# Optimization experiments

Hardware: AMD Instinct MI355X
Metric: run time of the kernel (lower is better)

The kernel has to match this reference:

```python
import jax, jax.numpy as jnp
import numpy as np

B, N, E = 4096, 64, 256      # graph pairs, nodes per drug, directed edges per drug
F, H, FP = 128, 64, 2048     # node feat dim, hidden dim, fingerprint dim


def setup_inputs() -> dict:
    key = jax.random.key(0)
    ks = jax.random.split(key, 14)
    return {
        "x1": jax.random.normal(ks[0], (B, N, F), jnp.float32),
        "x2": jax.random.normal(ks[1], (B, N, F), jnp.float32),
        "edge1": jax.random.randint(ks[2], (B, 2, E), 0, N, jnp.int32),
        "edge2": jax.random.randint(ks[3], (B, 2, E), 0, N, jnp.int32),
        "fp1": jax.random.uniform(ks[4], (B, FP), jnp.float32),
        "fp2": jax.random.uniform(ks[5], (B, FP), jnp.float32),
        "W1": jax.random.normal(ks[6], (F, H), jnp.float32) * 0.05,
        "b1": jnp.zeros((H,), jnp.float32),
        "W2": jax.random.normal(ks[7], (H, H), jnp.float32) * 0.05,
        "b2": jnp.zeros((H,), jnp.float32),
        "Wm1": jax.random.normal(ks[8], (2 * H + 2 * FP, 256), jnp.float32) * 0.02,
        "bm1": jnp.zeros((256,), jnp.float32),
        "Wm2": jax.random.normal(ks[9], (256, 1), jnp.float32) * 0.05,
        "bm2": jnp.zeros((1,), jnp.float32),
    }


def gcn_conv(x, src, dst, W, b):
    """PyG GCNConv: self-loops + symmetric normalization, aggregated at dst."""
    n = x.shape[0]
    loops = jnp.arange(n, dtype=src.dtype)
    s = jnp.concatenate([src, loops])
    d = jnp.concatenate([dst, loops])
    deg = jax.ops.segment_sum(jnp.ones_like(d, jnp.float32), d, num_segments=n)
    norm = jax.lax.rsqrt(deg)                      # deg >= 1 due to self-loops
    xw = x @ W                                     # [n, H]
    msg = xw[s] * (norm[s] * norm[d])[:, None]     # [n+E, H]
    return jax.ops.segment_sum(msg, d, num_segments=n) + b


def encode(x, edges, W1, b1, W2, b2):
    src, dst = edges[0], edges[1]
    h = jax.nn.relu(gcn_conv(x, src, dst, W1, b1))
    h = jax.nn.relu(gcn_conv(h, src, dst, W2, b2))
    return h.mean(axis=0)                          # global_mean_pool (1 graph)


_encode_b = jax.vmap(encode, in_axes=(0, 0, None, None, None, None))


def reference(x1, x2, edge1, edge2, fp1, fp2, W1, b1, W2, b2, Wm1, bm1, Wm2, bm2):
    h1 = _encode_b(x1, edge1, W1, b1, W2, b2)      # [B, H]
    h2 = _encode_b(x2, edge2, W1, b1, W2, b2)      # [B, H]
    fused = jnp.concatenate([h1, h2, fp1, fp2], axis=1)  # [B, 2H+2FP]
    hidden = jax.nn.relu(fused @ Wm1 + bm1)
    return jax.nn.sigmoid(hidden @ Wm2 + bm2).reshape(-1)
```

## Files before the change

kernel.cpp:

```cpp
#include <hip/hip_runtime.h>
#include <math.h>

#define B_PAIRS 4096
#define NNODES  64
#define NEDGES  256
#define FDIM    128
#define HDIM    64
#define FPDIM   2048
#define MDIM    256
#define KTOT    4224

typedef __attribute__((ext_vector_type(4))) float f32x4;
typedef __bf16 bf16x8 __attribute__((ext_vector_type(8)));

__device__ __forceinline__ unsigned short f2bf(float f) {
    return __builtin_bit_cast(unsigned short, (__bf16)f);
}
__device__ __forceinline__ unsigned pack2(float a, float b) {
    return (unsigned)f2bf(a) | ((unsigned)f2bf(b) << 16);
}
__device__ __forceinline__ unsigned long long pack4(float a, float b, float c, float d) {
    return (unsigned long long)pack2(a, b) | ((unsigned long long)pack2(c, d) << 32);
}

__global__ void prep_weights(const float* __restrict__ W1, const float* __restrict__ W2,
                             unsigned short* __restrict__ W1t, unsigned short* __restrict__ W2t) {
    const int t0 = blockIdx.x * 256 + threadIdx.x;
    const int stride = gridDim.x * 256;
    for (int i = t0; i < HDIM * FDIM; i += stride) {
        const int n = i >> 7, k = i & 127;
        W1t[i] = f2bf(W1[k * HDIM + n]);
    }
    for (int i = t0; i < HDIM * HDIM; i += stride) {
        const int n = i >> 6, k = i & 63;
        W2t[i] = f2bf(W2[k * HDIM + n]);
    }
}

__global__ __launch_bounds__(256)
void prep_wm1(const float* __restrict__ Wm1, unsigned short* __restrict__ Wm1t) {
    __shared__ float tile[32][33];
    const int k0 = blockIdx.x * 32, n0 = blockIdx.y * 32;
    const int t = threadIdx.x;
    const int c = t & 31, r8 = t >> 5;
    #pragma unroll
    for (int rr = r8; rr < 32; rr += 8)
        tile[rr][c] = Wm1[(size_t)(k0 + rr) * MDIM + n0 + c];
    __syncthreads();
    #pragma unroll
    for (int j = 0; j < 4; ++j) {
        const int n = n0 + r8 + 8 * j;
        Wm1t[(size_t)n * KTOT + k0 + c] = f2bf(tile[c][r8 + 8 * j]);
    }
}

#define WAITLDS() do { __asm__ volatile("s_waitcnt lgkmcnt(0)" ::: "memory"); \
                       __builtin_amdgcn_sched_barrier(0); } while (0)

__global__ __launch_bounds__(64, 2)
void encode_kernel(const float* __restrict__ x1, const float* __restrict__ x2,
                   const int* __restrict__ e1, const int* __restrict__ e2,
                   const unsigned short* __restrict__ W1t, const float* __restrict__ b1,
                   const unsigned short* __restrict__ W2t, const float* __restrict__ b2,
                   float* __restrict__ hbuf) {
    __shared__ __align__(16) unsigned char lds[17152];
    const int gid  = blockIdx.x;
    const int drug = gid >> 12;
    const int b    = gid & (B_PAIRS - 1);
    const float* x  = (drug ? x2 : x1) + (size_t)b * NNODES * FDIM;
    const int*   eg = (drug ? e2 : e1) + (size_t)b * 2 * NEDGES;

    const int t  = threadIdx.x;
    const int lr = t & 15, lg = t >> 4;
    const unsigned swl = (unsigned)(lr & 7) << 4;

    unsigned* cnt = (unsigned*)(lds + 8192);
    float*    nrm = (float*)(lds + 16640);
    int*      deg = (int*)(lds + 16896);

    float4 xalo[16];
    #pragma unroll
    for (int mt = 0; mt < 2; ++mt) {
        const float* xr = x + (size_t)(16 * mt + lr) * FDIM + 8 * lg;
        #pragma unroll
        for (int ks = 0; ks < 4; ++ks) {
            xalo[mt * 8 + 2 * ks]     = ((const float4*)(xr + 32 * ks))[0];
            xalo[mt * 8 + 2 * ks + 1] = ((const float4*)(xr + 32 * ks))[1];
        }
    }
    const int4 s4 = ((const int4*)eg)[t];
    const int4 d4 = ((const int4*)eg)[t + 64];

    #pragma unroll
    for (int i = 0; i < 8; ++i) ((uint4*)cnt)[t + 64 * i] = make_uint4(0, 0, 0, 0);
    if (t < 16) ((uint4*)cnt)[512 + t] = make_uint4(0, 0, 0, 0);
    deg[t] = 0;
    WAITLDS();

    {
        const int ss[4] = {s4.x, s4.y, s4.z, s4.w};
        const int dd[4] = {d4.x, d4.y, d4.z, d4.w};
        #pragma unroll
        for (int i = 0; i < 4; ++i) {
            atomicAdd(&deg[dd[i]], 1);
            atomicAdd(&cnt[dd[i] * 33 + (ss[i] >> 1)], 1u << ((ss[i] & 1) * 16));
        }
    }
    WAITLDS();

    float4 xahi[16];
    #pragma unroll
    for (int mt = 0; mt < 2; ++mt) {
        const float* xr = x + (size_t)(16 * (mt + 2) + lr) * FDIM + 8 * lg;
        #pragma unroll
        for (int ks = 0; ks < 4; ++ks) {
            xahi[mt * 8 + 2 * ks]     = ((const float4*)(xr + 32 * ks))[0];
            xahi[mt * 8 + 2 * ks + 1] = ((const float4*)(xr + 32 * ks))[1];
        }
    }

    nrm[t] = rsqrtf((float)deg[t] + 1.0f);
    WAITLDS();

    bf16x8 bw1[16];
    #pragma unroll
    for (int nt = 0; nt < 4; ++nt)
        #pragma unroll
        for (int ks = 0; ks < 4; ++ks)
            bw1[nt * 4 + ks] = *(const bf16x8*)(W1t + (16 * nt + lr) * FDIM + 32 * ks + 8 * lg);

    {
        const int r = t;
        const float nr = nrm[r];
        unsigned char* arow = lds + r * 128;
        const unsigned sw = (unsigned)(r & 7) << 4;
        #pragma unroll
        for (int cw = 0; cw < 16; ++cw) {
            const unsigned w0 = cnt[r * 33 + 2 * cw];
            const unsigned w1 = cnt[r * 33 + 2 * cw + 1];
            const float4 nv = ((const float4*)nrm)[cw];
            const int c = 4 * cw;
            const float u0 = (float)((w0 & 0xffffu) + (r == c     ? 1u : 0u)) * nr * nv.x;
            const float u1 = (float)((w0 >> 16)     + (r == c + 1 ? 1u : 0u)) * nr * nv.y;
            const float u2 = (float)((w1 & 0xffffu) + (r == c + 2 ? 1u : 0u)) * nr * nv.z;
            const float u3 = (float)((w1 >> 16)     + (r == c + 3 ? 1u : 0u)) * nr * nv.w;
            *(unsigned long long*)(arow + (((unsigned)(8 * cw)) ^ sw)) = pack4(u0, u1, u2, u3);
        }
    }
    WAITLDS();

    #pragma unroll
    for (int half = 0; half < 2; ++half) {
        const float4* xs = half ? xahi : xalo;
        #pragma unroll
        for (int m2i = 0; m2i < 2; ++m2i) {
            const int mt = half * 2 + m2i;
            f32x4 acc[4];
            #pragma unroll
            for (int nt = 0; nt < 4; ++nt) acc[nt] = (f32x4){0.f, 0.f, 0.f, 0.f};
            #pragma unroll
            for (int ks = 0; ks < 4; ++ks) {
                bf16x8 a;
                const float4 u = xs[m2i * 8 + 2 * ks], v = xs[m2i * 8 + 2 * ks + 1];
                a[0] = (__bf16)u.x; a[1] = (__bf16)u.y; a[2] = (__bf16)u.z; a[3] = (__bf16)u.w;
                a[4] = (__bf16)v.x; a[5] = (__bf16)v.y; a[6] = (__bf16)v.z; a[7] = (__bf16)v.w;
                #pragma unroll
                for (int nt = 0; nt < 4; ++nt)
                    acc[nt] = __builtin_amdgcn_mfma_f32_16x16x32_bf16(a, bw1[nt * 4 + ks], acc[nt], 0, 0, 0);
            }
            const unsigned m2 = (unsigned)(2 * (16 * mt + 4 * lg));
            #pragma unroll
            for (int nt = 0; nt < 4; ++nt) {
                const int f = 16 * nt + lr;
                *(unsigned long long*)(lds + 8192u + (unsigned)f * 128 + (m2 ^ swl)) =
                    pack4(acc[nt][0], acc[nt][1], acc[nt][2], acc[nt][3]);
            }
        }
    }
    WAITLDS();

    {
        bf16x8 ta[8], ba[8];
        #pragma unroll
        for (int mt = 0; mt < 4; ++mt)
            #pragma unroll
            for (int ks = 0; ks < 2; ++ks)
                ta[mt * 2 + ks] = *(const bf16x8*)(lds + 8192u + (unsigned)(16 * mt + lr) * 128 +
                                                   (((unsigned)(64 * ks + 16 * lg)) ^ swl));
        #pragma unroll
        for (int nt = 0; nt < 4; ++nt)
            #pragma unroll
            for (int ks = 0; ks < 2; ++ks)
                ba[nt * 2 + ks] = *(const bf16x8*)(lds + (unsigned)(16 * nt + lr) * 128 +
                                                   (((unsigned)(64 * ks + 16 * lg)) ^ swl));
        WAITLDS();
        #pragma unroll
        for (int mt = 0; mt < 4; ++mt) {
            f32x4 acc[4];
            #pragma unroll
            for (int nt = 0; nt < 4; ++nt) acc[nt] = (f32x4){0.f, 0.f, 0.f, 0.f};
            #pragma unroll
            for (int ks = 0; ks < 2; ++ks) {
                #pragma unroll
                for (int nt = 0; nt < 4; ++nt)
                    acc[nt] = __builtin_amdgcn_mfma_f32_16x16x32_bf16(ta[mt * 2 + ks], ba[nt * 2 + ks], acc[nt], 0, 0, 0);
            }
            const int m0 = 16 * mt + 4 * lg;
            const float4 b1v = *(const float4*)(b1 + m0);
            const unsigned m2 = (unsigned)(2 * m0);
            #pragma unroll
            for (int nt = 0; nt < 4; ++nt) {
                const int d = 16 * nt + lr;
                const float v0 = fmaxf(acc[nt][0] + b1v.x, 0.f);
                const float v1 = fmaxf(acc[nt][1] + b1v.y, 0.f);
                const float v2 = fmaxf(acc[nt][2] + b1v.z, 0.f);
                const float v3 = fmaxf(acc[nt][3] + b1v.w, 0.f);
                *(unsigned long long*)(lds + 8192u + (unsigned)d * 128 + (m2 ^ swl)) =
                    pack4(v0, v1, v2, v3);
            }
        }
    }
    WAITLDS();

    {
        bf16x8 ta[8], bw2[8];
        #pragma unroll
        for (int mt = 0; mt < 4; ++mt)
            #pragma unroll
            for (int ks = 0; ks < 2; ++ks)
                ta[mt * 2 + ks] = *(const bf16x8*)(lds + 8192u + (unsigned)(16 * mt + lr) * 128 +
                                                   (((unsigned)(64 * ks + 16 * lg)) ^ swl));
        #pragma unroll
        for (int nt = 0; nt < 4; ++nt)
            #pragma unroll
            for (int ks = 0; ks < 2; ++ks)
                bw2[nt * 2 + ks] = *(const bf16x8*)(W2t + (16 * nt + lr) * HDIM + 32 * ks + 8 * lg);
        WAITLDS();
        #pragma unroll
        for (int mt = 0; mt < 4; ++mt) {
            f32x4 acc[4];
            #pragma unroll
            for (int nt = 0; nt < 4; ++nt) acc[nt] = (f32x4){0.f, 0.f, 0.f, 0.f};
            #pragma unroll
            for (int ks = 0; ks < 2; ++ks) {
                #pragma unroll
                for (int nt = 0; nt < 4; ++nt)
                    acc[nt] = __builtin_amdgcn_mfma_f32_16x16x32_bf16(ta[mt * 2 + ks], bw2[nt * 2 + ks], acc[nt], 0, 0, 0);
            }
            const unsigned m2 = (unsigned)(2 * (16 * mt + 4 * lg));
            #pragma unroll
            for (int nt = 0; nt < 4; ++nt) {
                const int n = 16 * nt + lr;
                *(unsigned long long*)(lds + 8192u + (unsigned)n * 128 + (m2 ^ swl)) =
                    pack4(acc[nt][0], acc[nt][1], acc[nt][2], acc[nt][3]);
            }
        }
    }
    WAITLDS();

    {
        bf16x8 bt3[8];
        #pragma unroll
        for (int nt = 0; nt < 4; ++nt)
            #pragma unroll
            for (int ks = 0; ks < 2; ++ks)
                bt3[nt * 2 + ks] = *(const bf16x8*)(lds + 8192u + (unsigned)(16 * nt + lr) * 128 +
                                                    (((unsigned)(64 * ks + 16 * lg)) ^ swl));
        float b2v[4], p[4];
        #pragma unroll
        for (int nt = 0; nt < 4; ++nt) { b2v[nt] = b2[16 * nt + lr]; p[nt] = 0.f; }
        #pragma unroll
        for (int mt = 0; mt < 4; ++mt) {
            f32x4 acc[4];
            #pragma unroll
            for (int nt = 0; nt < 4; ++nt) acc[nt] = (f32x4){0.f, 0.f, 0.f, 0.f};
            #pragma unroll
            for (int ks = 0; ks < 2; ++ks) {
                const bf16x8 a = *(const bf16x8*)(lds + (unsigned)(16 * mt + lr) * 128 +
                                                  (((unsigned)(64 * ks + 16 * lg)) ^ swl));
                #pragma unroll
                for (int nt = 0; nt < 4; ++nt)
                    acc[nt] = __builtin_amdgcn_mfma_f32_16x16x32_bf16(a, bt3[nt * 2 + ks], acc[nt], 0, 0, 0);
            }
            #pragma unroll
            for (int nt = 0; nt < 4; ++nt) {
                #pragma unroll
                for (int j = 0; j < 4; ++j) p[nt] += fmaxf(acc[nt][j] + b2v[nt], 0.f);
            }
        }
        #pragma unroll
        for (int nt = 0; nt < 4; ++nt) {
            p[nt] += __shfl_xor(p[nt], 16, 64);
            p[nt] += __shfl_xor(p[nt], 32, 64);
        }
        if (lg == 0) {
            float* hout = hbuf + ((size_t)drug * B_PAIRS + b) * HDIM;
            #pragma unroll
            for (int nt = 0; nt < 4; ++nt) hout[16 * nt + lr] = p[nt] * (1.0f / 64.0f);
        }
    }
}

__global__ __launch_bounds__(256)
void fused_mlp_kernel(const float* __restrict__ fp1, const float* __restrict__ fp2,
                      const float* __restrict__ hbuf,
                      const unsigned short* __restrict__ Wm1t,
                      const float* __restrict__ bm1, const float* __restrict__ Wm2,
                      const float* __restrict__ bm2, float* __restrict__ out) {
    __shared__ __align__(16) unsigned char lds[8448];
    float* pool = (float*)(lds + 8192);
    const int t = threadIdx.x;
    const int lane = t & 63, wid = t >> 6;
    const int lr = lane & 15, lg = lane >> 4;
    const int pair0 = blockIdx.x * 16;

    const int r  = t >> 4;
    const int kc = (t & 15) << 3;
    const int pr = pair0 + r;
    const unsigned wOff = (unsigned)r * 256 + (((unsigned)(2 * kc)) ^ ((unsigned)(r & 7) << 4));

    f32x4 acc[4];
    #pragma unroll
    for (int nf = 0; nf < 4; ++nf) acc[nf] = (f32x4){0.f, 0.f, 0.f, 0.f};

    const unsigned short* brow[4];
    #pragma unroll
    for (int nf = 0; nf < 4; ++nf)
        brow[nf] = Wm1t + (size_t)(64 * wid + 16 * nf + lr) * KTOT + 8 * lg;

    float4 va, vb;
    #define LOAD_A(s)                                                                  \
        {                                                                              \
            const float* src;                                                          \
            if ((s) == 0)                                                              \
                src = (kc < 64) ? hbuf + (size_t)pr * HDIM + kc                        \
                                : hbuf + (size_t)(B_PAIRS + pr) * HDIM + (kc - 64);    \
            else if ((s) <= 16)                                                        \
                src = fp1 + (size_t)pr * FPDIM + ((s) - 1) * 128 + kc;                 \
            else                                                                       \
                src = fp2 + (size_t)pr * FPDIM + ((s) - 17) * 128 + kc;                \
            va = ((const float4*)src)[0];                                              \
            vb = ((const float4*)src)[1];                                              \
        }
    #define STORE_A(base)                                                              \
        *(uint4*)((base) + wOff) = make_uint4(pack2(va.x, va.y), pack2(va.z, va.w),    \
                                              pack2(vb.x, vb.y), pack2(vb.z, vb.w));

    LOAD_A(0);
    STORE_A(lds);
    for (int s = 0; s < 33; ++s) {
        const bool more = (s + 1 < 33);
        if (more) LOAD_A(s + 1);
        __syncthreads();
        const unsigned char* buf = lds + (unsigned)((s & 1) << 12);
        const unsigned asw = (unsigned)(lr & 7) << 4;
        const int kglob = s << 7;
        #pragma unroll
        for (int ks = 0; ks < 4; ++ks) {
            const unsigned kb = (unsigned)(64 * ks + 16 * lg);
            const bf16x8 a = *(const bf16x8*)(buf + (unsigned)lr * 256 + (kb ^ asw));
            #pragma unroll
            for (int nf = 0; nf < 4; ++nf) {
                const bf16x8 bw = *(const bf16x8*)(brow[nf] + kglob + 32 * ks);
                acc[nf] = __builtin_amdgcn_mfma_f32_16x16x32_bf16(a, bw, acc[nf], 0, 0, 0);
            }
        }
        if (more) STORE_A(lds + (unsigned)(((s + 1) & 1) << 12));
    }

    float bm1v[4], wm2v[4];
    #pragma unroll
    for (int nf = 0; nf < 4; ++nf) {
        const int n = 64 * wid + 16 * nf + lr;
        bm1v[nf] = bm1[n];
        wm2v[nf] = Wm2[n];
    }
    #pragma unroll
    for (int reg = 0; reg < 4; ++reg) {
        float p = 0.f;
        #pragma unroll
        for (int nf = 0; nf < 4; ++nf)
            p += fmaxf(acc[nf][reg] + bm1v[nf], 0.f) * wm2v[nf];
        p += __shfl_xor(p, 1, 64);
        p += __shfl_xor(p, 2, 64);
        p += __shfl_xor(p, 4, 64);
        p += __shfl_xor(p, 8, 64);
        if (lr == 0) pool[wid * 16 + 4 * lg + reg] = p;
    }
    __syncthreads();
    if (t < 16) {
        const float y = pool[t] + pool[16 + t] + pool[32 + t] + pool[48 + t] + bm2[0];
        out[pair0 + t] = 1.0f / (1.0f + expf(-y));
    }
    #undef LOAD_A
    #undef STORE_A
}

extern "C" void kernel_launch(void* const* d_in, const int* in_sizes, int n_in,
                              void* d_out, int out_size, void* d_ws, size_t ws_size,
                              hipStream_t stream) {
    const float* x1  = (const float*)d_in[0];
    const float* x2  = (const float*)d_in[1];
    const int*   e1  = (const int*)d_in[2];
    const int*   e2  = (const int*)d_in[3];
    const float* fp1 = (const float*)d_in[4];
    const float* fp2 = (const float*)d_in[5];
    const float* W1  = (const float*)d_in[6];
    const float* b1  = (const float*)d_in[7];
    const float* W2  = (const float*)d_in[8];
    const float* b2  = (const float*)d_in[9];
    const float* Wm1 = (const float*)d_in[10];
    const float* bm1 = (const float*)d_in[11];
    const float* Wm2 = (const float*)d_in[12];
    const float* bm2 = (const float*)d_in[13];
    float* out  = (float*)d_out;

    float* hbuf = (float*)d_ws;
    unsigned short* W1t  = (unsigned short*)((char*)d_ws + (2 << 20));
    unsigned short* W2t  = W1t + HDIM * FDIM;
    unsigned short* Wm1t = (unsigned short*)((char*)d_ws + (3 << 20));

    hipLaunchKernelGGL(prep_weights, dim3(16), dim3(256), 0, stream, W1, W2, W1t, W2t);
    hipLaunchKernelGGL(prep_wm1, dim3(132, 8), dim3(256), 0, stream, Wm1, Wm1t);
    hipLaunchKernelGGL(encode_kernel, dim3(2 * B_PAIRS), dim3(64), 0, stream,
                       x1, x2, e1, e2, W1t, b1, W2t, b2, hbuf);
    hipLaunchKernelGGL(fused_mlp_kernel, dim3(B_PAIRS / 16), dim3(256), 0, stream,
                       fp1, fp2, hbuf, Wm1t, bm1, Wm2, bm2, out);
}
```

Baseline: 162.3 us.

## Process four graphs per encode block with software-prefetched node features

The encode kernel becomes persistent-ish: each 64-thread block loops over four graphs instead of one, hoisting W2/b2 loads out of the loop. While the current graph is computed, the next graph's node features and edge lists are prefetched into registers, so global load latency overlaps with MFMA and LDS work. The cost is fewer blocks (2048 instead of 8192), which lowers parallelism and latency hiding across waves, plus higher register pressure from the double-buffered feature registers under launch_bounds(64,2).

```diff
diff --git a/kernel.cpp b/kernel.cpp
--- a/kernel.cpp
+++ b/kernel.cpp
@@ -9,6 +9,7 @@
 #define FPDIM   2048
 #define MDIM    256
 #define KTOT    4224
+#define GPW     4
 
 typedef __attribute__((ext_vector_type(4))) float f32x4;
 typedef __bf16 bf16x8 __attribute__((ext_vector_type(8)));
@@ -21,6 +22,12 @@
 }
 __device__ __forceinline__ unsigned long long pack4(float a, float b, float c, float d) {
     return (unsigned long long)pack2(a, b) | ((unsigned long long)pack2(c, d) << 32);
+}
+__device__ __forceinline__ bf16x8 cvt8(float4 u, float4 v) {
+    bf16x8 a;
+    a[0] = (__bf16)u.x; a[1] = (__bf16)u.y; a[2] = (__bf16)u.z; a[3] = (__bf16)u.w;
+    a[4] = (__bf16)v.x; a[5] = (__bf16)v.y; a[6] = (__bf16)v.z; a[7] = (__bf16)v.w;
+    return a;
 }
 
 __global__ void prep_weights(const float* __restrict__ W1, const float* __restrict__ W2,
@@ -64,12 +71,6 @@
                    const unsigned short* __restrict__ W2t, const float* __restrict__ b2,
                    float* __restrict__ hbuf) {
     __shared__ __align__(16) unsigned char lds[17152];
-    const int gid  = blockIdx.x;
-    const int drug = gid >> 12;
-    const int b    = gid & (B_PAIRS - 1);
-    const float* x  = (drug ? x2 : x1) + (size_t)b * NNODES * FDIM;
-    const int*   eg = (drug ? e2 : e1) + (size_t)b * 2 * NEDGES;
-
     const int t  = threadIdx.x;
     const int lr = t & 15, lg = t >> 4;
     const unsigned swl = (unsigned)(lr & 7) << 4;
@@ -78,96 +79,137 @@
     float*    nrm = (float*)(lds + 16640);
     int*      deg = (int*)(lds + 16896);
 
-    float4 xalo[16];
-    #pragma unroll
-    for (int mt = 0; mt < 2; ++mt) {
-        const float* xr = x + (size_t)(16 * mt + lr) * FDIM + 8 * lg;
-        #pragma unroll
-        for (int ks = 0; ks < 4; ++ks) {
-            xalo[mt * 8 + 2 * ks]     = ((const float4*)(xr + 32 * ks))[0];
-            xalo[mt * 8 + 2 * ks + 1] = ((const float4*)(xr + 32 * ks))[1];
-        }
-    }
-    const int4 s4 = ((const int4*)eg)[t];
-    const int4 d4 = ((const int4*)eg)[t + 64];
-
-    #pragma unroll
-    for (int i = 0; i < 8; ++i) ((uint4*)cnt)[t + 64 * i] = make_uint4(0, 0, 0, 0);
-    if (t < 16) ((uint4*)cnt)[512 + t] = make_uint4(0, 0, 0, 0);
-    deg[t] = 0;
-    WAITLDS();
-
+    const int g0 = blockIdx.x * GPW;
+
+    bf16x8 bw2[8];
+    #pragma unroll
+    for (int nt = 0; nt < 4; ++nt)
+        #pragma unroll
+        for (int ks = 0; ks < 2; ++ks)
+            bw2[nt * 2 + ks] = *(const bf16x8*)(W2t + (16 * nt + lr) * HDIM + 32 * ks + 8 * lg);
+    float b2v[4];
+    #pragma unroll
+    for (int nt = 0; nt < 4; ++nt) b2v[nt] = b2[16 * nt + lr];
+
+    float4 xaA[16], xaB[16];
+    int4 s4, d4;
     {
-        const int ss[4] = {s4.x, s4.y, s4.z, s4.w};
-        const int dd[4] = {d4.x, d4.y, d4.z, d4.w};
-        #pragma unroll
-        for (int i = 0; i < 4; ++i) {
-            atomicAdd(&deg[dd[i]], 1);
-            atomicAdd(&cnt[dd[i] * 33 + (ss[i] >> 1)], 1u << ((ss[i] & 1) * 16));
-        }
-    }
-    WAITLDS();
-
-    float4 xahi[16];
-    #pragma unroll
-    for (int mt = 0; mt < 2; ++mt) {
-        const float* xr = x + (size_t)(16 * (mt + 2) + lr) * FDIM + 8 * lg;
-        #pragma unroll
-        for (int ks = 0; ks < 4; ++ks) {
-            xahi[mt * 8 + 2 * ks]     = ((const float4*)(xr + 32 * ks))[0];
-            xahi[mt * 8 + 2 * ks + 1] = ((const float4*)(xr + 32 * ks))[1];
-        }
-    }
-
-    nrm[t] = rsqrtf((float)deg[t] + 1.0f);
-    WAITLDS();
-
-    bf16x8 bw1[16];
-    #pragma unroll
-    for (int nt = 0; nt < 4; ++nt)
-        #pragma unroll
-        for (int ks = 0; ks < 4; ++ks)
-            bw1[nt * 4 + ks] = *(const bf16x8*)(W1t + (16 * nt + lr) * FDIM + 32 * ks + 8 * lg);
-
-    {
-        const int r = t;
-        const float nr = nrm[r];
-        unsigned char* arow = lds + r * 128;
-        const unsigned sw = (unsigned)(r & 7) << 4;
-        #pragma unroll
-        for (int cw = 0; cw < 16; ++cw) {
-            const unsigned w0 = cnt[r * 33 + 2 * cw];
-            const unsigned w1 = cnt[r * 33 + 2 * cw + 1];
-            const float4 nv = ((const float4*)nrm)[cw];
-            const int c = 4 * cw;
-            const float u0 = (float)((w0 & 0xffffu) + (r == c     ? 1u : 0u)) * nr * nv.x;
-            const float u1 = (float)((w0 >> 16)     + (r == c + 1 ? 1u : 0u)) * nr * nv.y;
-            const float u2 = (float)((w1 & 0xffffu) + (r == c + 2 ? 1u : 0u)) * nr * nv.z;
-            const float u3 = (float)((w1 >> 16)     + (r == c + 3 ? 1u : 0u)) * nr * nv.w;
-            *(unsigned long long*)(arow + (((unsigned)(8 * cw)) ^ sw)) = pack4(u0, u1, u2, u3);
-        }
-    }
-    WAITLDS();
-
-    #pragma unroll
-    for (int half = 0; half < 2; ++half) {
-        const float4* xs = half ? xahi : xalo;
-        #pragma unroll
-        for (int m2i = 0; m2i < 2; ++m2i) {
-            const int mt = half * 2 + m2i;
+        const int gid = g0;
+        const float* x = ((gid >> 12) ? x2 : x1) + (size_t)(gid & (B_PAIRS - 1)) * NNODES * FDIM;
+        #pragma unroll
+        for (int mt = 0; mt < 2; ++mt) {
+            const float* xr = x + (size_t)(16 * mt + lr) * FDIM + 8 * lg;
+            #pragma unroll
+            for (int ks = 0; ks < 4; ++ks) {
+                xaA[mt * 8 + 2 * ks]     = ((const float4*)(xr + 32 * ks))[0];
+                xaA[mt * 8 + 2 * ks + 1] = ((const float4*)(xr + 32 * ks))[1];
+            }
+            const float* xr2 = x + (size_t)(16 * (mt + 2) + lr) * FDIM + 8 * lg;
+            #pragma unroll
+            for (int ks = 0; ks < 4; ++ks) {
+                xaB[mt * 8 + 2 * ks]     = ((const float4*)(xr2 + 32 * ks))[0];
+                xaB[mt * 8 + 2 * ks + 1] = ((const float4*)(xr2 + 32 * ks))[1];
+            }
+        }
+        const int* eg = ((gid >> 12) ? e2 : e1) + (size_t)(gid & (B_PAIRS - 1)) * 2 * NEDGES;
+        s4 = ((const int4*)eg)[t];
+        d4 = ((const int4*)eg)[t + 64];
+    }
+
+    #pragma unroll 1
+    for (int it = 0; it < GPW; ++it) {
+        const int gid  = g0 + it;
+        const int drug = gid >> 12;
+        const int b    = gid & (B_PAIRS - 1);
+        const bool more = (it + 1 < GPW);
+        const int gn   = gid + 1;
+        const float* xn = ((gn >> 12) ? x2 : x1) + (size_t)(gn & (B_PAIRS - 1)) * NNODES * FDIM;
+        const int*  egn = ((gn >> 12) ? e2 : e1) + (size_t)(gn & (B_PAIRS - 1)) * 2 * NEDGES;
+
+        #pragma unroll
+        for (int i = 0; i < 8; ++i) ((uint4*)cnt)[t + 64 * i] = make_uint4(0, 0, 0, 0);
+        if (t < 16) ((uint4*)cnt)[512 + t] = make_uint4(0, 0, 0, 0);
+        deg[t] = 0;
+        WAITLDS();
+
+        {
+            const int ss[4] = {s4.x, s4.y, s4.z, s4.w};
+            const int dd[4] = {d4.x, d4.y, d4.z, d4.w};
+            #pragma unroll
+            for (int i = 0; i < 4; ++i) {
+                atomicAdd(&deg[dd[i]], 1);
+                atomicAdd(&cnt[dd[i] * 33 + (ss[i] >> 1)], 1u << ((ss[i] & 1) * 16));
+            }
+        }
+        WAITLDS();
+        nrm[t] = rsqrtf((float)deg[t] + 1.0f);
+        WAITLDS();
+
+        bf16x8 bw1[16];
+        #pragma unroll
+        for (int nt = 0; nt < 4; ++nt)
+            #pragma unroll
+            for (int ks = 0; ks < 4; ++ks)
+                bw1[nt * 4 + ks] = *(const bf16x8*)(W1t + (16 * nt + lr) * FDIM + 32 * ks + 8 * lg);
+
+        {
+            const int r = t;
+            const float nr = nrm[r];
+            unsigned char* arow = lds + r * 128;
+            const unsigned sw = (unsigned)(r & 7) << 4;
+            #pragma unroll
+            for (int cw = 0; cw < 16; ++cw) {
+                const unsigned w0 = cnt[r * 33 + 2 * cw];
+                const unsigned w1 = cnt[r * 33 + 2 * cw + 1];
+                const float4 nv = ((const float4*)nrm)[cw];
+                const int c = 4 * cw;
+                const float u0 = (float)((w0 & 0xffffu) + (r == c     ? 1u : 0u)) * nr * nv.x;
+                const float u1 = (float)((w0 >> 16)     + (r == c + 1 ? 1u : 0u)) * nr * nv.y;
+                const float u2 = (float)((w1 & 0xffffu) + (r == c + 2 ? 1u : 0u)) * nr * nv.z;
+                const float u3 = (float)((w1 >> 16)     + (r == c + 3 ? 1u : 0u)) * nr * nv.w;
+                *(unsigned long long*)(arow + (((unsigned)(8 * cw)) ^ sw)) = pack4(u0, u1, u2, u3);
+            }
+        }
+        WAITLDS();
+
+        bf16x8 xb[16];
+        #pragma unroll
+        for (int mt = 0; mt < 2; ++mt)
+            #pragma unroll
+            for (int ks = 0; ks < 4; ++ks)
+                xb[mt * 4 + ks] = cvt8(xaA[mt * 8 + 2 * ks], xaA[mt * 8 + 2 * ks + 1]);
+        if (more) {
+            #pragma unroll
+            for (int mt = 0; mt < 2; ++mt) {
+                const float* xr = xn + (size_t)(16 * mt + lr) * FDIM + 8 * lg;
+                #pragma unroll
+                for (int ks = 0; ks < 4; ++ks) {
+                    xaA[mt * 8 + 2 * ks]     = ((const float4*)(xr + 32 * ks))[0];
+                    xaA[mt * 8 + 2 * ks + 1] = ((const float4*)(xr + 32 * ks))[1];
+                }
+            }
+        }
+        #pragma unroll
+        for (int mt = 0; mt < 2; ++mt)
+            #pragma unroll
+            for (int ks = 0; ks < 4; ++ks)
+                xb[(mt + 2) * 4 + ks] = cvt8(xaB[mt * 8 + 2 * ks], xaB[mt * 8 + 2 * ks + 1]);
+        int4 s4n, d4n;
+        if (more) {
+            s4n = ((const int4*)egn)[t];
+            d4n = ((const int4*)egn)[t + 64];
+        }
+
+        #pragma unroll
+        for (int mt = 0; mt < 4; ++mt) {
             f32x4 acc[4];
             #pragma unroll
             for (int nt = 0; nt < 4; ++nt) acc[nt] = (f32x4){0.f, 0.f, 0.f, 0.f};
             #pragma unroll
-            for (int ks = 0; ks < 4; ++ks) {
-                bf16x8 a;
-                const float4 u = xs[m2i * 8 + 2 * ks], v = xs[m2i * 8 + 2 * ks + 1];
-                a[0] = (__bf16)u.x; a[1] = (__bf16)u.y; a[2] = (__bf16)u.z; a[3] = (__bf16)u.w;
-                a[4] = (__bf16)v.x; a[5] = (__bf16)v.y; a[6] = (__bf16)v.z; a[7] = (__bf16)v.w;
+            for (int ks = 0; ks < 4; ++ks)
                 #pragma unroll
                 for (int nt = 0; nt < 4; ++nt)
-                    acc[nt] = __builtin_amdgcn_mfma_f32_16x16x32_bf16(a, bw1[nt * 4 + ks], acc[nt], 0, 0, 0);
-            }
+                    acc[nt] = __builtin_amdgcn_mfma_f32_16x16x32_bf16(xb[mt * 4 + ks], bw1[nt * 4 + ks], acc[nt], 0, 0, 0);
             const unsigned m2 = (unsigned)(2 * (16 * mt + 4 * lg));
             #pragma unroll
             for (int nt = 0; nt < 4; ++nt) {
@@ -176,128 +218,134 @@
                     pack4(acc[nt][0], acc[nt][1], acc[nt][2], acc[nt][3]);
             }
         }
-    }
-    WAITLDS();
-
-    {
-        bf16x8 ta[8], ba[8];
-        #pragma unroll
-        for (int mt = 0; mt < 4; ++mt)
-            #pragma unroll
-            for (int ks = 0; ks < 2; ++ks)
-                ta[mt * 2 + ks] = *(const bf16x8*)(lds + 8192u + (unsigned)(16 * mt + lr) * 128 +
-                                                   (((unsigned)(64 * ks + 16 * lg)) ^ swl));
-        #pragma unroll
-        for (int nt = 0; nt < 4; ++nt)
-            #pragma unroll
-            for (int ks = 0; ks < 2; ++ks)
-                ba[nt * 2 + ks] = *(const bf16x8*)(lds + (unsigned)(16 * nt + lr) * 128 +
-                                                   (((unsigned)(64 * ks + 16 * lg)) ^ swl));
-        WAITLDS();
-        #pragma unroll
-        for (int mt = 0; mt < 4; ++mt) {
-            f32x4 acc[4];
-            #pragma unroll
-            for (int nt = 0; nt < 4; ++nt) acc[nt] = (f32x4){0.f, 0.f, 0.f, 0.f};
-            #pragma unroll
-            for (int ks = 0; ks < 2; ++ks) {
-                #pragma unroll
-                for (int nt = 0; nt < 4; ++nt)
-                    acc[nt] = __builtin_amdgcn_mfma_f32_16x16x32_bf16(ta[mt * 2 + ks], ba[nt * 2 + ks], acc[nt], 0, 0, 0);
-            }
-            const int m0 = 16 * mt + 4 * lg;
-            const float4 b1v = *(const float4*)(b1 + m0);
-            const unsigned m2 = (unsigned)(2 * m0);
+        WAITLDS();
+
+        if (more) {
+            #pragma unroll
+            for (int mt = 0; mt < 2; ++mt) {
+                const float* xr2 = xn + (size_t)(16 * (mt + 2) + lr) * FDIM + 8 * lg;
+                #pragma unroll
+                for (int ks = 0; ks < 4; ++ks) {
+                    xaB[mt * 8 + 2 * ks]     = ((const float4*)(xr2 + 32 * ks))[0];
+                    xaB[mt * 8 + 2 * ks + 1] = ((const float4*)(xr2 + 32 * ks))[1];
+                }
+            }
+        }
+
+        {
+            bf16x8 ta[8], ba[8];
+            #pragma unroll
+            for (int mt = 0; mt < 4; ++mt)
+                #pragma unroll
+                for (int ks = 0; ks < 2; ++ks)
+                    ta[mt * 2 + ks] = *(const bf16x8*)(lds + 8192u + (unsigned)(16 * mt + lr) * 128 +
+                                                       (((unsigned)(64 * ks + 16 * lg)) ^ swl));
+            #pragma unroll
+            for (int nt = 0; nt < 4; ++nt)
+                #pragma unroll
+                for (int ks = 0; ks < 2; ++ks)
+                    ba[nt * 2 + ks] = *(const bf16x8*)(lds + (unsigned)(16 * nt + lr) * 128 +
+                                                       (((unsigned)(64 * ks + 16 * lg)) ^ swl));
+            WAITLDS();
+            #pragma unroll
+            for (int mt = 0; mt < 4; ++mt) {
+                f32x4 acc[4];
+                #pragma unroll
+                for (int nt = 0; nt < 4; ++nt) acc[nt] = (f32x4){0.f, 0.f, 0.f, 0.f};
+                #pragma unroll
+                for (int ks = 0; ks < 2; ++ks)
+                    #pragma unroll
+                    for (int nt = 0; nt < 4; ++nt)
+                        acc[nt] = __builtin_amdgcn_mfma_f32_16x16x32_bf16(ta[mt * 2 + ks], ba[nt * 2 + ks], acc[nt], 0, 0, 0);
+                const int m0 = 16 * mt + 4 * lg;
+                const float4 b1v = *(const float4*)(b1 + m0);
+                const unsigned m2 = (unsigned)(2 * m0);
+                #pragma unroll
+                for (int nt = 0; nt < 4; ++nt) {
+                    const int d = 16 * nt + lr;
+                    const float v0 = fmaxf(acc[nt][0] + b1v.x, 0.f);
+                    const float v1 = fmaxf(acc[nt][1] + b1v.y, 0.f);
+                    const float v2 = fmaxf(acc[nt][2] + b1v.z, 0.f);
+                    const float v3 = fmaxf(acc[nt][3] + b1v.w, 0.f);
+                    *(unsigned long long*)(lds + 8192u + (unsigned)d * 128 + (m2 ^ swl)) =
+                        pack4(v0, v1, v2, v3);
+                }
+            }
+        }
+        WAITLDS();
+
+        {
+            bf16x8 ta[8];
+            #pragma unroll
+            for (int mt = 0; mt < 4; ++mt)
+                #pragma unroll
+                for (int ks = 0; ks < 2; ++ks)
+                    ta[mt * 2 + ks] = *(const bf16x8*)(lds + 8192u + (unsigned)(16 * mt + lr) * 128 +
+                                                       (((unsigned)(64 * ks + 16 * lg)) ^ swl));
+            WAITLDS();
+            #pragma unroll
+            for (int mt = 0; mt < 4; ++mt) {
+                f32x4 acc[4];
+                #pragma unroll
+                for (int nt = 0; nt < 4; ++nt) acc[nt] = (f32x4){0.f, 0.f, 0.f, 0.f};
+                #pragma unroll
+                for (int ks = 0; ks < 2; ++ks)
+                    #pragma unroll
+                    for (int nt = 0; nt < 4; ++nt)
+                        acc[nt] = __builtin_amdgcn_mfma_f32_16x16x32_bf16(ta[mt * 2 + ks], bw2[nt * 2 + ks], acc[nt], 0, 0, 0);
+                const unsigned m2 = (unsigned)(2 * (16 * mt + 4 * lg));
+                #pragma unroll
+                for (int nt = 0; nt < 4; ++nt) {
+                    const int n = 16 * nt + lr;
+                    *(unsigned long long*)(lds + 8192u + (unsigned)n * 128 + (m2 ^ swl)) =
+                        pack4(acc[nt][0], acc[nt][1], acc[nt][2], acc[nt][3]);
+                }
+            }
+        }
+        WAITLDS();
+
+        {
+            bf16x8 bt3[8];
+            #pragma unroll
+            for (int nt = 0; nt < 4; ++nt)
+                #pragma unroll
+                for (int ks = 0; ks < 2; ++ks)
+                    bt3[nt * 2 + ks] = *(const bf16x8*)(lds + 8192u + (unsigned)(16 * nt + lr) * 128 +
+                                                        (((unsigned)(64 * ks + 16 * lg)) ^ swl));
+            float p[4];
+            #pragma unroll
+            for (int nt = 0; nt < 4; ++nt) p[nt] = 0.f;
+            #pragma unroll
+            for (int mt = 0; mt < 4; ++mt) {
+                f32x4 acc[4];
+                #pragma unroll
+                for (int nt = 0; nt < 4; ++nt) acc[nt] = (f32x4){0.f, 0.f, 0.f, 0.f};
+                #pragma unroll
+                for (int ks = 0; ks < 2; ++ks) {
+                    const bf16x8 a = *(const bf16x8*)(lds + (unsigned)(16 * mt + lr) * 128 +
+                                                      (((unsigned)(64 * ks + 16 * lg)) ^ swl));
+                    #pragma unroll
+                    for (int nt = 0; nt < 4; ++nt)
+                        acc[nt] = __builtin_amdgcn_mfma_f32_16x16x32_bf16(a, bt3[nt * 2 + ks], acc[nt], 0, 0, 0);
+                }
+                #pragma unroll
+                for (int nt = 0; nt < 4; ++nt) {
+                    #pragma unroll
+                    for (int j = 0; j < 4; ++j) p[nt] += fmaxf(acc[nt][j] + b2v[nt], 0.f);
+                }
+            }
             #pragma unroll
             for (int nt = 0; nt < 4; ++nt) {
-                const int d = 16 * nt + lr;
-                const float v0 = fmaxf(acc[nt][0] + b1v.x, 0.f);
-                const float v1 = fmaxf(acc[nt][1] + b1v.y, 0.f);
-                const float v2 = fmaxf(acc[nt][2] + b1v.z, 0.f);
-                const float v3 = fmaxf(acc[nt][3] + b1v.w, 0.f);
-                *(unsigned long long*)(lds + 8192u + (unsigned)d * 128 + (m2 ^ swl)) =
-                    pack4(v0, v1, v2, v3);
-            }
-        }
-    }
-    WAITLDS();
-
-    {
-        bf16x8 ta[8], bw2[8];
-        #pragma unroll
-        for (int mt = 0; mt < 4; ++mt)
-            #pragma unroll
-            for (int ks = 0; ks < 2; ++ks)
-                ta[mt * 2 + ks] = *(const bf16x8*)(lds + 8192u + (unsigned)(16 * mt + lr) * 128 +
-                                                   (((unsigned)(64 * ks + 16 * lg)) ^ swl));
-        #pragma unroll
-        for (int nt = 0; nt < 4; ++nt)
-            #pragma unroll
-            for (int ks = 0; ks < 2; ++ks)
-                bw2[nt * 2 + ks] = *(const bf16x8*)(W2t + (16 * nt + lr) * HDIM + 32 * ks + 8 * lg);
-        WAITLDS();
-        #pragma unroll
-        for (int mt = 0; mt < 4; ++mt) {
-            f32x4 acc[4];
-            #pragma unroll
-            for (int nt = 0; nt < 4; ++nt) acc[nt] = (f32x4){0.f, 0.f, 0.f, 0.f};
-            #pragma unroll
-            for (int ks = 0; ks < 2; ++ks) {
-                #pragma unroll
-                for (int nt = 0; nt < 4; ++nt)
-                    acc[nt] = __builtin_amdgcn_mfma_f32_16x16x32_bf16(ta[mt * 2 + ks], bw2[nt * 2 + ks], acc[nt], 0, 0, 0);
-            }
-            const unsigned m2 = (unsigned)(2 * (16 * mt + 4 * lg));
-            #pragma unroll
-            for (int nt = 0; nt < 4; ++nt) {
-                const int n = 16 * nt + lr;
-                *(unsigned long long*)(lds + 8192u + (unsigned)n * 128 + (m2 ^ swl)) =
-                    pack4(acc[nt][0], acc[nt][1], acc[nt][2], acc[nt][3]);
-            }
-        }
-    }
-    WAITLDS();
-
-    {
-        bf16x8 bt3[8];
-        #pragma unroll
-        for (int nt = 0; nt < 4; ++nt)
-            #pragma unroll
-            for (int ks = 0; ks < 2; ++ks)
-                bt3[nt * 2 + ks] = *(const bf16x8*)(lds + 8192u + (unsigned)(16 * nt + lr) * 128 +
-                                                    (((unsigned)(64 * ks + 16 * lg)) ^ swl));
-        float b2v[4], p[4];
-        #pragma unroll
-        for (int nt = 0; nt < 4; ++nt) { b2v[nt] = b2[16 * nt + lr]; p[nt] = 0.f; }
-        #pragma unroll
-        for (int mt = 0; mt < 4; ++mt) {
-            f32x4 acc[4];
-            #pragma unroll
-            for (int nt = 0; nt < 4; ++nt) acc[nt] = (f32x4){0.f, 0.f, 0.f, 0.f};
-            #pragma unroll
-            for (int ks = 0; ks < 2; ++ks) {
-                const bf16x8 a = *(const bf16x8*)(lds + (unsigned)(16 * mt + lr) * 128 +
-                                                  (((unsigned)(64 * ks + 16 * lg)) ^ swl));
-                #pragma unroll
-                for (int nt = 0; nt < 4; ++nt)
-                    acc[nt] = __builtin_amdgcn_mfma_f32_16x16x32_bf16(a, bt3[nt * 2 + ks], acc[nt], 0, 0, 0);
-            }
-            #pragma unroll
-            for (int nt = 0; nt < 4; ++nt) {
-                #pragma unroll
-                for (int j = 0; j < 4; ++j) p[nt] += fmaxf(acc[nt][j] + b2v[nt], 0.f);
-            }
-        }
-        #pragma unroll
-        for (int nt = 0; nt < 4; ++nt) {
-            p[nt] += __shfl_xor(p[nt], 16, 64);
-            p[nt] += __shfl_xor(p[nt], 32, 64);
-        }
-        if (lg == 0) {
-            float* hout = hbuf + ((size_t)drug * B_PAIRS + b) * HDIM;
-            #pragma unroll
-            for (int nt = 0; nt < 4; ++nt) hout[16 * nt + lr] = p[nt] * (1.0f / 64.0f);
-        }
+                p[nt] += __shfl_xor(p[nt], 16, 64);
+                p[nt] += __shfl_xor(p[nt], 32, 64);
+            }
+            if (lg == 0) {
+                float* hout = hbuf + ((size_t)drug * B_PAIRS + b) * HDIM;
+                #pragma unroll
+                for (int nt = 0; nt < 4; ++nt) hout[16 * nt + lr] = p[nt] * (1.0f / 64.0f);
+            }
+        }
+        if (more) { s4 = s4n; d4 = d4n; }
     }
 }
 
@@ -422,7 +470,7 @@
 
     hipLaunchKernelGGL(prep_weights, dim3(16), dim3(256), 0, stream, W1, W2, W1t, W2t);
     hipLaunchKernelGGL(prep_wm1, dim3(132, 8), dim3(256), 0, stream, Wm1, Wm1t);
-    hipLaunchKernelGGL(encode_kernel, dim3(2 * B_PAIRS), dim3(64), 0, stream,
+    hipLaunchKernelGGL(encode_kernel, dim3(2 * B_PAIRS / GPW), dim3(64), 0, stream,
                        x1, x2, e1, e2, W1t, b1, W2t, b2, hbuf);
     hipLaunchKernelGGL(fused_mlp_kernel, dim3(B_PAIRS / 16), dim3(256), 0, stream,
                        fp1, fp2, hbuf, Wm1t, bm1, Wm2, bm2, out);
```

After: 282.8 us. 1.74x slower.

## Keep normalized adjacency in registers as MFMA fragments and shrink LDS

Applied to the files above, without the earlier changes.

The normalized adjacency matrix is now built directly into bf16x8 MFMA operand registers (ahat) from the edge-count table, so it is no longer written to LDS and read back before each aggregation. Both aggregation GEMMs reuse those registers, which removes the LDS round trips and lets the count table share space with the activation buffer. Total shared memory drops from about 17 KB to about 9 KB per block. The trade-off is that the eight extra live vector registers raise register pressure, which could limit occupancy under the launch bounds. Because the matrix is symmetric-normalized, the same fragment serves as the A and B operand in different stages.

```diff
diff --git a/kernel.cpp b/kernel.cpp
--- a/kernel.cpp
+++ b/kernel.cpp
@@ -63,7 +63,7 @@
                    const unsigned short* __restrict__ W1t, const float* __restrict__ b1,
                    const unsigned short* __restrict__ W2t, const float* __restrict__ b2,
                    float* __restrict__ hbuf) {
-    __shared__ __align__(16) unsigned char lds[17152];
+    __shared__ __align__(16) unsigned char lds[8960];
     const int gid  = blockIdx.x;
     const int drug = gid >> 12;
     const int b    = gid & (B_PAIRS - 1);
@@ -74,9 +74,9 @@
     const int lr = t & 15, lg = t >> 4;
     const unsigned swl = (unsigned)(lr & 7) << 4;
 
-    unsigned* cnt = (unsigned*)(lds + 8192);
-    float*    nrm = (float*)(lds + 16640);
-    int*      deg = (int*)(lds + 16896);
+    unsigned* cnt = (unsigned*)lds;
+    float*    nrm = (float*)(lds + 8448);
+    int*      deg = (int*)(lds + 8704);
 
     float4 xalo[16];
     #pragma unroll
@@ -111,11 +111,11 @@
     float4 xahi[16];
     #pragma unroll
     for (int mt = 0; mt < 2; ++mt) {
-        const float* xr = x + (size_t)(16 * (mt + 2) + lr) * FDIM + 8 * lg;
+        const float* xr2 = x + (size_t)(16 * (mt + 2) + lr) * FDIM + 8 * lg;
         #pragma unroll
         for (int ks = 0; ks < 4; ++ks) {
-            xahi[mt * 8 + 2 * ks]     = ((const float4*)(xr + 32 * ks))[0];
-            xahi[mt * 8 + 2 * ks + 1] = ((const float4*)(xr + 32 * ks))[1];
+            xahi[mt * 8 + 2 * ks]     = ((const float4*)(xr2 + 32 * ks))[0];
+            xahi[mt * 8 + 2 * ks + 1] = ((const float4*)(xr2 + 32 * ks))[1];
         }
     }
 
@@ -129,22 +129,33 @@
         for (int ks = 0; ks < 4; ++ks)
             bw1[nt * 4 + ks] = *(const bf16x8*)(W1t + (16 * nt + lr) * FDIM + 32 * ks + 8 * lg);
 
+    bf16x8 ahat[8];
     {
-        const int r = t;
-        const float nr = nrm[r];
-        unsigned char* arow = lds + r * 128;
-        const unsigned sw = (unsigned)(r & 7) << 4;
-        #pragma unroll
-        for (int cw = 0; cw < 16; ++cw) {
-            const unsigned w0 = cnt[r * 33 + 2 * cw];
-            const unsigned w1 = cnt[r * 33 + 2 * cw + 1];
-            const float4 nv = ((const float4*)nrm)[cw];
-            const int c = 4 * cw;
-            const float u0 = (float)((w0 & 0xffffu) + (r == c     ? 1u : 0u)) * nr * nv.x;
-            const float u1 = (float)((w0 >> 16)     + (r == c + 1 ? 1u : 0u)) * nr * nv.y;
-            const float u2 = (float)((w1 & 0xffffu) + (r == c + 2 ? 1u : 0u)) * nr * nv.z;
-            const float u3 = (float)((w1 >> 16)     + (r == c + 3 ? 1u : 0u)) * nr * nv.w;
-            *(unsigned long long*)(arow + (((unsigned)(8 * cw)) ^ sw)) = pack4(u0, u1, u2, u3);
+        const float ncol[2][8] = {
+            { nrm[8 * lg + 0], nrm[8 * lg + 1], nrm[8 * lg + 2], nrm[8 * lg + 3],
+              nrm[8 * lg + 4], nrm[8 * lg + 5], nrm[8 * lg + 6], nrm[8 * lg + 7] },
+            { nrm[32 + 8 * lg + 0], nrm[32 + 8 * lg + 1], nrm[32 + 8 * lg + 2], nrm[32 + 8 * lg + 3],
+              nrm[32 + 8 * lg + 4], nrm[32 + 8 * lg + 5], nrm[32 + 8 * lg + 6], nrm[32 + 8 * lg + 7] }
+        };
+        #pragma unroll
+        for (int q = 0; q < 4; ++q) {
+            const int r = 16 * q + lr;
+            const float nr = nrm[r];
+            #pragma unroll
+            for (int ks = 0; ks < 2; ++ks) {
+                const int c0 = 32 * ks + 8 * lg;
+                const uint4 w = *(const uint4*)(cnt + r * 33 + (c0 >> 1));
+                const unsigned ww[4] = { w.x, w.y, w.z, w.w };
+                bf16x8 f;
+                #pragma unroll
+                for (int e = 0; e < 8; ++e) {
+                    const int c = c0 + e;
+                    const unsigned m = (e & 1) ? (ww[e >> 1] >> 16) : (ww[e >> 1] & 0xffffu);
+                    const float v = (float)(m + (r == c ? 1u : 0u)) * nr * ncol[ks][e];
+                    f[e] = (__bf16)v;
+                }
+                ahat[q * 2 + ks] = f;
+            }
         }
     }
     WAITLDS();
@@ -172,7 +183,7 @@
             #pragma unroll
             for (int nt = 0; nt < 4; ++nt) {
                 const int f = 16 * nt + lr;
-                *(unsigned long long*)(lds + 8192u + (unsigned)f * 128 + (m2 ^ swl)) =
+                *(unsigned long long*)(lds + (unsigned)f * 128 + (m2 ^ swl)) =
                     pack4(acc[nt][0], acc[nt][1], acc[nt][2], acc[nt][3]);
             }
         }
@@ -180,18 +191,12 @@
     WAITLDS();
 
     {
-        bf16x8 ta[8], ba[8];
+        bf16x8 ta[8];
         #pragma unroll
         for (int mt = 0; mt < 4; ++mt)
             #pragma unroll
             for (int ks = 0; ks < 2; ++ks)
-                ta[mt * 2 + ks] = *(const bf16x8*)(lds + 8192u + (unsigned)(16 * mt + lr) * 128 +
-                                                   (((unsigned)(64 * ks + 16 * lg)) ^ swl));
-        #pragma unroll
-        for (int nt = 0; nt < 4; ++nt)
-            #pragma unroll
-            for (int ks = 0; ks < 2; ++ks)
-                ba[nt * 2 + ks] = *(const bf16x8*)(lds + (unsigned)(16 * nt + lr) * 128 +
+                ta[mt * 2 + ks] = *(const bf16x8*)(lds + (unsigned)(16 * mt + lr) * 128 +
                                                    (((unsigned)(64 * ks + 16 * lg)) ^ swl));
         WAITLDS();
         #pragma unroll
@@ -200,11 +205,10 @@
             #pragma unroll
             for (int nt = 0; nt < 4; ++nt) acc[nt] = (f32x4){0.f, 0.f, 0.f, 0.f};
             #pragma unroll
-            for (int ks = 0; ks < 2; ++ks) {
+            for (int ks = 0; ks < 2; ++ks)
                 #pragma unroll
                 for (int nt = 0; nt < 4; ++nt)
-                    acc[nt] = __builtin_amdgcn_mfma_f32_16x16x32_bf16(ta[mt * 2 + ks], ba[nt * 2 + ks], acc[nt], 0, 0, 0);
-            }
+                    acc[nt] = __builtin_amdgcn_mfma_f32_16x16x32_bf16(ta[mt * 2 + ks], ahat[nt * 2 + ks], acc[nt], 0, 0, 0);
             const int m0 = 16 * mt + 4 * lg;
             const float4 b1v = *(const float4*)(b1 + m0);
             const unsigned m2 = (unsigned)(2 * m0);
@@ -215,7 +219,7 @@
                 const float v1 = fmaxf(acc[nt][1] + b1v.y, 0.f);
                 const float v2 = fmaxf(acc[nt][2] + b1v.z, 0.f);
                 const float v3 = fmaxf(acc[nt][3] + b1v.w, 0.f);
-                *(unsigned long long*)(lds + 8192u + (unsigned)d * 128 + (m2 ^ swl)) =
+                *(unsigned long long*)(lds + (unsigned)d * 128 + (m2 ^ swl)) =
                     pack4(v0, v1, v2, v3);
             }
         }
@@ -228,7 +232,7 @@
         for (int mt = 0; mt < 4; ++mt)
             #pragma unroll
             for (int ks = 0; ks < 2; ++ks)
-                ta[mt * 2 + ks] = *(const bf16x8*)(lds + 8192u + (unsigned)(16 * mt + lr) * 128 +
+                ta[mt * 2 + ks] = *(const bf16x8*)(lds + (unsigned)(16 * mt + lr) * 128 +
                                                    (((unsigned)(64 * ks + 16 * lg)) ^ swl));
         #pragma unroll
         for (int nt = 0; nt < 4; ++nt)
@@ -242,16 +246,15 @@
             #pragma unroll
             for (int nt = 0; nt < 4; ++nt) acc[nt] = (f32x4){0.f, 0.f, 0.f, 0.f};
             #pragma unroll
-            for (int ks = 0; ks < 2; ++ks) {
+            for (int ks = 0; ks < 2; ++ks)
                 #pragma unroll
                 for (int nt = 0; nt < 4; ++nt)
                     acc[nt] = __builtin_amdgcn_mfma_f32_16x16x32_bf16(ta[mt * 2 + ks], bw2[nt * 2 + ks], acc[nt], 0, 0, 0);
-            }
             const unsigned m2 = (unsigned)(2 * (16 * mt + 4 * lg));
             #pragma unroll
             for (int nt = 0; nt < 4; ++nt) {
                 const int n = 16 * nt + lr;
-                *(unsigned long long*)(lds + 8192u + (unsigned)n * 128 + (m2 ^ swl)) =
+                *(unsigned long long*)(lds + (unsigned)n * 128 + (m2 ^ swl)) =
                     pack4(acc[nt][0], acc[nt][1], acc[nt][2], acc[nt][3]);
             }
         }
@@ -264,7 +267,7 @@
         for (int nt = 0; nt < 4; ++nt)
             #pragma unroll
             for (int ks = 0; ks < 2; ++ks)
-                bt3[nt * 2 + ks] = *(const bf16x8*)(lds + 8192u + (unsigned)(16 * nt + lr) * 128 +
+                bt3[nt * 2 + ks] = *(const bf16x8*)(lds + (unsigned)(16 * nt + lr) * 128 +
                                                     (((unsigned)(64 * ks + 16 * lg)) ^ swl));
         float b2v[4], p[4];
         #pragma unroll
@@ -275,13 +278,10 @@
             #pragma unroll
             for (int nt = 0; nt < 4; ++nt) acc[nt] = (f32x4){0.f, 0.f, 0.f, 0.f};
             #pragma unroll
-            for (int ks = 0; ks < 2; ++ks) {
-                const bf16x8 a = *(const bf16x8*)(lds + (unsigned)(16 * mt + lr) * 128 +
-                                                  (((unsigned)(64 * ks + 16 * lg)) ^ swl));
+            for (int ks = 0; ks < 2; ++ks)
                 #pragma unroll
                 for (int nt = 0; nt < 4; ++nt)
-                    acc[nt] = __builtin_amdgcn_mfma_f32_16x16x32_bf16(a, bt3[nt * 2 + ks], acc[nt], 0, 0, 0);
-            }
+                    acc[nt] = __builtin_amdgcn_mfma_f32_16x16x32_bf16(ahat[mt * 2 + ks], bt3[nt * 2 + ks], acc[nt], 0, 0, 0);
             #pragma unroll
             for (int nt = 0; nt < 4; ++nt) {
                 #pragma unroll
```

Result: no change. 160.8 us (median of 2 runs) (-0.9%).
